# Performance work log

Hardware: AMD Instinct MI355X
Metric: run time of the kernel (lower is better)

Reference implementation:

```python
import jax, jax.numpy as jnp
import numpy as np

DIM = 512
HEADS = 8
DIM_HEAD = 64
H_DIM = HEADS * DIM_HEAD  # 512
SCALE = DIM_HEAD ** -0.5


def setup_inputs() -> dict:
    key = jax.random.key(0)
    k_x, k_qkv, k_out, k_b = jax.random.split(key, 4)
    N, C, L = 4, DIM, 2048
    x = jax.random.normal(k_x, (N, C, L), dtype=jnp.float32)
    # Conv1d kernel_size=1 weights, kernel dim squeezed: [out_ch, in_ch]
    w_qkv = jax.random.normal(k_qkv, (3 * H_DIM, DIM), dtype=jnp.float32) * (DIM ** -0.5)
    w_out = jax.random.normal(k_out, (DIM, H_DIM), dtype=jnp.float32) * (H_DIM ** -0.5)
    b_out = jax.random.normal(k_b, (DIM,), dtype=jnp.float32) * 0.01
    return {"x": x, "w_qkv": w_qkv, "w_out": w_out, "b_out": b_out}


def reference(x, w_qkv, w_out, b_out):
    N, C, L = x.shape
    # 1x1 conv == pointwise linear over channels
    qkv = jnp.einsum('oc,ncl->nol', w_qkv, x)            # N, 3*h_dim, L
    q, k, v = jnp.split(qkv, 3, axis=1)                  # each N, h_dim, L
    # split heads: N, h, d, L
    q = q.reshape(N, HEADS, DIM_HEAD, L) * SCALE
    k = k.reshape(N, HEADS, DIM_HEAD, L)
    v = v.reshape(N, HEADS, DIM_HEAD, L)
    sim = jnp.einsum('nhdi,nhdj->nhij', q, k)            # N, h, L, L
    attn = jax.nn.softmax(sim, axis=-1)                  # stable softmax (max-subtract fused)
    out = jnp.einsum('nhij,nhdj->nhid', attn, v)         # N, h, L, d
    # 'b h l c -> b (h c) l'
    out = jnp.transpose(out, (0, 1, 3, 2)).reshape(N, H_DIM, L)
    return jnp.einsum('oc,ncl->nol', w_out, out) + b_out[None, :, None]
```

## Files before the change

kernel.cpp:

```cpp
#include <hip/hip_runtime.h>
#include <hip/hip_bf16.h>
#include <stdint.h>
#include <stddef.h>

typedef unsigned short u16;
typedef __bf16 bf16x8 __attribute__((ext_vector_type(8)));
typedef __bf16 bf16x2 __attribute__((ext_vector_type(2)));
typedef float f32x4 __attribute__((ext_vector_type(4)));
typedef unsigned short u16x8 __attribute__((ext_vector_type(8)));
typedef unsigned short u16x4 __attribute__((ext_vector_type(4)));

#define NBATCH 4
#define LSEQ   2048
#define CDIM   512
#define NHEADS 8
#define DHEAD  64
#define QSCALE 0.18033688011112042f

__device__ __forceinline__ float exp2_hw(float x) {
  return __builtin_amdgcn_exp2f(x);
}

__device__ __forceinline__ u16 f2bf(float f) {
  union { float f; unsigned u; } v; v.f = f;
  return (u16)((v.u + 0x7FFFu + ((v.u >> 16) & 1u)) >> 16);
}
__device__ __forceinline__ u16 f2bf_hw(float f) {
  union { __bf16 b; u16 u; } cv; cv.b = (__bf16)f; return cv.u;
}
__device__ __forceinline__ unsigned pack2bf(float a, float b) {
  union { bf16x2 v; unsigned u; } cv;
  cv.v[0] = (__bf16)a; cv.v[1] = (__bf16)b;
  return cv.u;
}
__device__ __forceinline__ f32x4 mfma16(bf16x8 a, bf16x8 b, f32x4 c) {
  return __builtin_amdgcn_mfma_f32_16x16x32_bf16(a, b, c, 0, 0, 0);
}
__device__ __forceinline__ void async16(const u16* gp, const u16* lp) {
  auto* g = reinterpret_cast<const __attribute__((address_space(1))) uint32_t*>(
      reinterpret_cast<uintptr_t>(gp));
  auto* l = reinterpret_cast<__attribute__((address_space(3))) uint32_t*>(
      reinterpret_cast<uintptr_t>(lp));
  __builtin_amdgcn_global_load_lds(g, l, 16, 0, 0);
}

__global__ __launch_bounds__(256) void prep(const float* __restrict__ x,
                                            const float* __restrict__ wqkv,
                                            const float* __restrict__ wout,
                                            u16* __restrict__ xT,
                                            u16* __restrict__ wqkvb,
                                            u16* __restrict__ woutb) {
  __shared__ u16 tile[32][36];
  int b = blockIdx.x, t = threadIdx.x;
  if (b < 4096) {
    int lb = b & 63, cb = (b >> 6) & 15, n = b >> 10;
    int c = t >> 3, lq = (t & 7) * 4;
    float4 f = *(const float4*)(x + ((size_t)(n * CDIM + cb * 32 + c)) * LSEQ + lb * 32 + lq);
    u16x4 cv;
    cv[0] = f2bf(f.x); cv[1] = f2bf(f.y); cv[2] = f2bf(f.z); cv[3] = f2bf(f.w);
    *(u16x4*)&tile[c][lq] = cv;
    __syncthreads();
    int l = t >> 3, cq = (t & 7) * 4;
    u16x4 o;
    o[0] = tile[cq + 0][l]; o[1] = tile[cq + 1][l];
    o[2] = tile[cq + 2][l]; o[3] = tile[cq + 3][l];
    *(u16x4*)(xT + ((size_t)(n * LSEQ + lb * 32 + l)) * CDIM + cb * 32 + cq) = o;
  } else {
    int i = (b - 4096) * 256 + t;
    const float4* src;
    u16* dst;
    int idx;
    if (i < 196608) { src = (const float4*)wqkv; dst = wqkvb; idx = i; }
    else            { src = (const float4*)wout; dst = woutb; idx = i - 196608; }
    float4 f = src[idx];
    u16x4 o;
    o[0] = f2bf(f.x); o[1] = f2bf(f.y); o[2] = f2bf(f.z); o[3] = f2bf(f.w);
    *(u16x4*)(dst + (size_t)idx * 4) = o;
  }
}

__global__ __launch_bounds__(256, 3) void qkv_gemm(const u16* __restrict__ wqkvb,
                                                   const u16* __restrict__ xT,
                                                   u16* __restrict__ qT,
                                                   u16* __restrict__ kT,
                                                   u16* __restrict__ vp) {
  __shared__ __align__(16) u16 lds[17408];
  u16* At = lds;
  u16* Bt = lds + 8192;

  int mb = blockIdx.x, lb = blockIdx.y, n = blockIdx.z;
  int o0 = mb * 128, l0 = lb * 128;
  int t = threadIdx.x, w = t >> 6, lane = t & 63, quad = lane >> 4, l15 = lane & 15;
  int wr = w >> 1, wc = w & 1;
  int lr = lane >> 3, lc = lane & 7;
  int swzS = (lc ^ lr) * 8;
  int swzR = l15 & 7;

  const u16* ag = wqkvb + (size_t)(o0 + w * 32 + lr) * CDIM + swzS;
  const u16* bg = xT + ((size_t)n * LSEQ + l0 + w * 32 + lr) * CDIM + swzS;

  f32x4 acc[4][4];
#pragma unroll
  for (int i = 0; i < 4; ++i)
#pragma unroll
    for (int j = 0; j < 4; ++j) acc[i][j] = (f32x4)0.0f;

  for (int k0 = 0; k0 < CDIM; k0 += 64) {
#pragma unroll
    for (int g = 0; g < 4; ++g) {
      async16(ag + (size_t)g * 8 * CDIM + k0, At + (w * 32 + g * 8) * 64);
      async16(bg + (size_t)g * 8 * CDIM + k0, Bt + (w * 32 + g * 8) * 64);
    }
    __syncthreads();
    bf16x8 af[4][2], bf[4][2];
#pragma unroll
    for (int rt = 0; rt < 4; ++rt)
#pragma unroll
      for (int kk = 0; kk < 2; ++kk) {
        af[rt][kk] = *(const bf16x8*)&At[(wr * 64 + rt * 16 + l15) * 64 +
                                         (((kk * 4 + quad) ^ swzR) * 8)];
        bf[rt][kk] = *(const bf16x8*)&Bt[(wc * 64 + rt * 16 + l15) * 64 +
                                         (((kk * 4 + quad) ^ swzR) * 8)];
      }
#pragma unroll
    for (int kk = 0; kk < 2; ++kk)
#pragma unroll
      for (int rt = 0; rt < 4; ++rt)
#pragma unroll
        for (int ct = 0; ct < 4; ++ct)
          acc[rt][ct] = mfma16(af[rt][kk], bf[ct][kk], acc[rt][ct]);
    __syncthreads();
  }

  int seg = mb >> 2;
  int hb = (mb & 3) * 2;
  if (seg < 2) {
    float scale = (seg == 0) ? QSCALE : 1.0f;
#pragma unroll
    for (int rt = 0; rt < 4; ++rt)
#pragma unroll
      for (int ct = 0; ct < 4; ++ct) {
        u16x4 ov;
#pragma unroll
        for (int r = 0; r < 4; ++r) ov[r] = f2bf_hw(acc[rt][ct][r] * scale);
        *(u16x4*)&lds[(wc * 64 + ct * 16 + l15) * 136 + wr * 64 + rt * 16 + quad * 4] = ov;
      }
    __syncthreads();
    u16* dst0 = (seg == 0) ? qT : kT;
#pragma unroll
    for (int p = 0; p < 8; ++p) {
      int l = p * 16 + (t >> 4);
      int ch = t & 15;
      u16x8 val = *(const u16x8*)&lds[l * 136 + ch * 8];
      int h = hb + (ch >> 3);
      int d = (ch & 7) * 8;
      *(u16x8*)(dst0 + (((size_t)(n * NHEADS + h)) * LSEQ + l0 + l) * DHEAD + d) = val;
    }
  } else {
#pragma unroll
    for (int rt = 0; rt < 4; ++rt)
#pragma unroll
      for (int ct = 0; ct < 4; ++ct)
#pragma unroll
        for (int r = 0; r < 4; ++r)
          lds[(wr * 64 + rt * 16 + quad * 4 + r) * 136 + wc * 64 + ct * 16 + l15] =
              f2bf_hw(acc[rt][ct][r]);
    __syncthreads();
#pragma unroll
    for (int p = 0; p < 8; ++p) {
      int o = p * 16 + (t >> 4);
      int ch = t & 15;
      u16x8 val = *(const u16x8*)&lds[o * 136 + ch * 8];
      int h = hb + (o >> 6);
      int d = o & 63;
      *(u16x8*)(vp + (((size_t)(n * NHEADS + h)) * DHEAD + d) * LSEQ + l0 + ch * 8) = val;
    }
  }
}

__global__ __launch_bounds__(256, 2) void attn_kernel(const u16* __restrict__ qT,
                                                      const u16* __restrict__ kT,
                                                      const u16* __restrict__ vp,
                                                      u16* __restrict__ aoT) {
  __shared__ __align__(16) u16 KVs[3][8192];

  int ib = blockIdx.x, h = blockIdx.y, n = blockIdx.z;
  int i0 = ib * 128;
  const u16* qb = qT + ((size_t)(n * NHEADS + h)) * LSEQ * DHEAD;
  const u16* kb = kT + ((size_t)(n * NHEADS + h)) * LSEQ * DHEAD;
  const u16* vb = vp + ((size_t)(n * NHEADS + h)) * DHEAD * LSEQ;
  int t = threadIdx.x, w = t >> 6, lane = t & 63, quad = lane >> 4, l15 = lane & 15;
  int wi = w >> 1, wj = w & 1;

  bf16x8 qf[4][2];
#pragma unroll
  for (int it = 0; it < 4; ++it)
#pragma unroll
    for (int kk = 0; kk < 2; ++kk)
      qf[it][kk] = *(const bf16x8*)(qb + (size_t)(i0 + wi * 64 + it * 16 + l15) * DHEAD +
                                    kk * 32 + quad * 8);

  f32x4 Oc[4][4];
#pragma unroll
  for (int it = 0; it < 4; ++it)
#pragma unroll
    for (int dt = 0; dt < 4; ++dt) Oc[it][dt] = (f32x4)0.0f;
  float lsum[4] = {0.f, 0.f, 0.f, 0.f};

  int lr = lane >> 3, lc = lane & 7;
  int swz = lc ^ lr;
  const u16* kgl = kb + lr * DHEAD + swz * 8;
  const u16* vgl = vb + (size_t)lr * LSEQ + swz * 8;
  int swzK = l15 & 7;

  auto stage = [&](int j0, int b) {
#pragma unroll
    for (int s = 0; s < 2; ++s) {
      int g = s * 4 + w;
      async16(kgl + (size_t)j0 * DHEAD + g * 512, &KVs[b][g * 512]);
      async16(vgl + j0 + (size_t)g * 8 * LSEQ, &KVs[b][4096 + g * 512]);
    }
  };

  bf16x8 pf_c[4];
  bf16x8 vf_c[4];

  auto tile_body = [&](int tt, bool do_pv) {
    const u16* Kt = &KVs[tt % 3][0];
    const u16* Vt = &KVs[tt % 3][4096];

    bf16x8 kf[2][2];
#pragma unroll
    for (int jt = 0; jt < 2; ++jt)
#pragma unroll
      for (int kk = 0; kk < 2; ++kk)
        kf[jt][kk] = *(const bf16x8*)&Kt[(wj * 32 + 16 * jt + l15) * 64 +
                                         (((quad + 4 * kk) ^ swzK) * 8)];

    if (do_pv) {
#pragma unroll
      for (int it = 0; it < 4; ++it)
#pragma unroll
        for (int dt = 0; dt < 4; ++dt)
          Oc[it][dt] = mfma16(vf_c[dt], pf_c[it], Oc[it][dt]);
    }

    f32x4 st[4][2];
#pragma unroll
    for (int it = 0; it < 4; ++it)
#pragma unroll
      for (int jt = 0; jt < 2; ++jt) {
        f32x4 s = (f32x4)0.0f;
        s = mfma16(kf[jt][0], qf[it][0], s);
        s = mfma16(kf[jt][1], qf[it][1], s);
        st[it][jt] = s;
      }

#pragma unroll
    for (int dt = 0; dt < 4; ++dt)
      vf_c[dt] = *(const bf16x8*)&Vt[(16 * dt + l15) * 64 +
                                     (((wj * 4 + quad) ^ swzK) * 8)];

#pragma unroll
    for (int it = 0; it < 4; ++it) {
      unsigned wjh[2][2];
#pragma unroll
      for (int jt = 0; jt < 2; ++jt) {
        float p0 = exp2_hw(st[it][jt][0]);
        float p1 = exp2_hw(st[it][jt][1]);
        float p2 = exp2_hw(st[it][jt][2]);
        float p3 = exp2_hw(st[it][jt][3]);
        lsum[it] += (p0 + p1) + (p2 + p3);
        wjh[jt][0] = pack2bf(p0, p1);
        wjh[jt][1] = pack2bf(p2, p3);
      }
      unsigned a0 = wjh[0][0], b0 = wjh[1][0];
      unsigned a1 = wjh[0][1], b1 = wjh[1][1];
      asm volatile("v_permlane32_swap_b32 %0, %1" : "+v"(a0), "+v"(b0));
      asm volatile("v_permlane16_swap_b32 %0, %1" : "+v"(a0), "+v"(b0));
      asm volatile("v_permlane32_swap_b32 %0, %1" : "+v"(a1), "+v"(b1));
      asm volatile("v_permlane16_swap_b32 %0, %1" : "+v"(a1), "+v"(b1));
      union { unsigned u[4]; bf16x8 v; } cv;
      cv.u[0] = a0; cv.u[1] = a1; cv.u[2] = b0; cv.u[3] = b1;
      pf_c[it] = cv.v;
    }
  };

  stage(0, 0);
  stage(64, 1);

  asm volatile("s_waitcnt vmcnt(4)" ::: "memory");
  __builtin_amdgcn_s_barrier();
  __builtin_amdgcn_sched_barrier(0);
  stage(128, 2);
  tile_body(0, false);

  for (int tt = 1; tt < 31; ++tt) {
    asm volatile("s_waitcnt vmcnt(4)" ::: "memory");
    __builtin_amdgcn_s_barrier();
    __builtin_amdgcn_sched_barrier(0);
    if (tt + 2 < 32) stage((tt + 2) * 64, (tt + 2) % 3);
    tile_body(tt, true);
  }

  asm volatile("s_waitcnt vmcnt(0)" ::: "memory");
  __builtin_amdgcn_s_barrier();
  __builtin_amdgcn_sched_barrier(0);
  tile_body(31, true);

#pragma unroll
  for (int it = 0; it < 4; ++it)
#pragma unroll
    for (int dt = 0; dt < 4; ++dt)
      Oc[it][dt] = mfma16(vf_c[dt], pf_c[it], Oc[it][dt]);

#pragma unroll
  for (int it = 0; it < 4; ++it) {
    lsum[it] += __shfl_xor(lsum[it], 16, 64);
    lsum[it] += __shfl_xor(lsum[it], 32, 64);
  }
  __syncthreads();
  float* Os = (float*)&KVs[0][0];
  float* Ls = (float*)((char*)&KVs[0][0] + 40960);
  if (wj == 1) {
#pragma unroll
    for (int it = 0; it < 4; ++it) {
#pragma unroll
      for (int dt = 0; dt < 4; ++dt)
        *(f32x4*)&Os[((((wi * 4 + it) * 4 + dt) * 16) + l15) * 20 + 4 * quad] =
            Oc[it][dt];
      if (quad == 0) Ls[(wi * 4 + it) * 16 + l15] = lsum[it];
    }
  }
  __syncthreads();
  if (wj == 0) {
#pragma unroll
    for (int it = 0; it < 4; ++it) {
      float lt = lsum[it] + Ls[(wi * 4 + it) * 16 + l15];
      float inv = 1.0f / lt;
      int row = i0 + wi * 64 + it * 16 + l15;
#pragma unroll
      for (int dt = 0; dt < 4; ++dt) {
        f32x4 part = *(const f32x4*)&Os[((((wi * 4 + it) * 4 + dt) * 16) + l15) * 20 +
                                        4 * quad];
        u16x4 ov;
#pragma unroll
        for (int r = 0; r < 4; ++r)
          ov[r] = f2bf_hw((Oc[it][dt][r] + part[r]) * inv);
        *(u16x4*)(aoT + ((size_t)n * LSEQ + row) * CDIM + h * DHEAD + 16 * dt +
                  4 * quad) = ov;
      }
    }
  }
}

__global__ __launch_bounds__(256, 3) void out_gemm(const u16* __restrict__ woutb,
                                                   const u16* __restrict__ aoT,
                                                   const float* __restrict__ bout,
                                                   float* __restrict__ out) {
  __shared__ __align__(16) u16 lds[16384];
  u16* At = lds;
  u16* Bt = lds + 8192;

  int mb = blockIdx.x, lb = blockIdx.y, n = blockIdx.z;
  int o0 = mb * 128, l0 = lb * 128;
  int t = threadIdx.x, w = t >> 6, lane = t & 63, quad = lane >> 4, l15 = lane & 15;
  int wr = w >> 1, wc = w & 1;
  int lr = lane >> 3, lc = lane & 7;
  int swzS = (lc ^ lr) * 8;
  int swzR = l15 & 7;

  const u16* ag = woutb + (size_t)(o0 + w * 32 + lr) * CDIM + swzS;
  const u16* bg = aoT + ((size_t)n * LSEQ + l0 + w * 32 + lr) * CDIM + swzS;

  f32x4 acc[4][4];
#pragma unroll
  for (int i = 0; i < 4; ++i)
#pragma unroll
    for (int j = 0; j < 4; ++j) acc[i][j] = (f32x4)0.0f;

  for (int k0 = 0; k0 < CDIM; k0 += 64) {
#pragma unroll
    for (int g = 0; g < 4; ++g) {
      async16(ag + (size_t)g * 8 * CDIM + k0, At + (w * 32 + g * 8) * 64);
      async16(bg + (size_t)g * 8 * CDIM + k0, Bt + (w * 32 + g * 8) * 64);
    }
    __syncthreads();
    bf16x8 af[4][2], bf[4][2];
#pragma unroll
    for (int rt = 0; rt < 4; ++rt)
#pragma unroll
      for (int kk = 0; kk < 2; ++kk) {
        af[rt][kk] = *(const bf16x8*)&At[(wr * 64 + rt * 16 + l15) * 64 +
                                         (((kk * 4 + quad) ^ swzR) * 8)];
        bf[rt][kk] = *(const bf16x8*)&Bt[(wc * 64 + rt * 16 + l15) * 64 +
                                         (((kk * 4 + quad) ^ swzR) * 8)];
      }
#pragma unroll
    for (int kk = 0; kk < 2; ++kk)
#pragma unroll
      for (int rt = 0; rt < 4; ++rt)
#pragma unroll
        for (int ct = 0; ct < 4; ++ct)
          acc[rt][ct] = mfma16(af[rt][kk], bf[ct][kk], acc[rt][ct]);
    __syncthreads();
  }

#pragma unroll
  for (int rt = 0; rt < 4; ++rt) {
    int orow = o0 + wr * 64 + rt * 16 + quad * 4;
#pragma unroll
    for (int r = 0; r < 4; ++r) {
      float bb = bout[orow + r];
      float* orow_p = out + ((size_t)n * CDIM + orow + r) * LSEQ + l0 + wc * 64;
#pragma unroll
      for (int ct = 0; ct < 4; ++ct)
        orow_p[ct * 16 + l15] = acc[rt][ct][r] + bb;
    }
  }
}

extern "C" void kernel_launch(void* const* d_in, const int* in_sizes, int n_in,
                              void* d_out, int out_size, void* d_ws, size_t ws_size,
                              hipStream_t stream) {
  (void)in_sizes; (void)n_in; (void)out_size; (void)ws_size;
  const float* x    = (const float*)d_in[0];
  const float* wqkv = (const float*)d_in[1];
  const float* wout = (const float*)d_in[2];
  const float* bout = (const float*)d_in[3];

  char* ws = (char*)d_ws;
  u16* xT    = (u16*)(ws + 0);
  u16* wqkvb = (u16*)(ws + 8388608);
  u16* woutb = (u16*)(ws + 9961472);
  u16* qT    = (u16*)(ws + 10485760);
  u16* kT    = (u16*)(ws + 18874368);
  u16* vp    = (u16*)(ws + 27262976);
  u16* aoT   = (u16*)(ws + 35651584);

  hipLaunchKernelGGL(prep, dim3(5120), dim3(256), 0, stream, x, wqkv, wout, xT, wqkvb, woutb);
  hipLaunchKernelGGL(qkv_gemm, dim3(12, 16, 4), dim3(256), 0, stream, wqkvb, xT, qT, kT, vp);
  hipLaunchKernelGGL(attn_kernel, dim3(16, 8, 4), dim3(256), 0, stream, qT, kT, vp, aoT);
  hipLaunchKernelGGL(out_gemm, dim3(4, 16, 4), dim3(256), 0, stream, woutb, aoT, bout,
                     (float*)d_out);
}
```

Before: 148.5 us.

## Triple-buffer the output projection GEMM with async loads and manual waitcnt

The out_gemm K loop moves from a single LDS buffer with two barriers per step to a three-stage ring buffer. Global-to-LDS async loads for step ks+2 are issued while step ks computes, and explicit vmcnt waits plus a single barrier per step guard each buffer. This is meant to hide global load latency behind MFMA work. In exchange, LDS use per block triples and the launch-bounds occupancy hint is dropped, which may lower the number of resident blocks per CU.

```diff
diff --git a/kernel.cpp b/kernel.cpp
--- a/kernel.cpp
+++ b/kernel.cpp
@@ -354,13 +354,11 @@
   }
 }
 
-__global__ __launch_bounds__(256, 3) void out_gemm(const u16* __restrict__ woutb,
-                                                   const u16* __restrict__ aoT,
-                                                   const float* __restrict__ bout,
-                                                   float* __restrict__ out) {
-  __shared__ __align__(16) u16 lds[16384];
-  u16* At = lds;
-  u16* Bt = lds + 8192;
+__global__ __launch_bounds__(256) void out_gemm(const u16* __restrict__ woutb,
+                                                const u16* __restrict__ aoT,
+                                                const float* __restrict__ bout,
+                                                float* __restrict__ out) {
+  __shared__ __align__(16) u16 lds[49152];
 
   int mb = blockIdx.x, lb = blockIdx.y, n = blockIdx.z;
   int o0 = mb * 128, l0 = lb * 128;
@@ -379,13 +377,19 @@
 #pragma unroll
     for (int j = 0; j < 4; ++j) acc[i][j] = (f32x4)0.0f;
 
-  for (int k0 = 0; k0 < CDIM; k0 += 64) {
+  auto stage = [&](int ks, int b) {
+    u16* At = lds + b * 16384;
+    u16* Bt = At + 8192;
 #pragma unroll
     for (int g = 0; g < 4; ++g) {
-      async16(ag + (size_t)g * 8 * CDIM + k0, At + (w * 32 + g * 8) * 64);
-      async16(bg + (size_t)g * 8 * CDIM + k0, Bt + (w * 32 + g * 8) * 64);
-    }
-    __syncthreads();
+      async16(ag + (size_t)g * 8 * CDIM + ks * 64, At + (w * 32 + g * 8) * 64);
+      async16(bg + (size_t)g * 8 * CDIM + ks * 64, Bt + (w * 32 + g * 8) * 64);
+    }
+  };
+
+  auto body = [&](int ks) {
+    const u16* At = lds + (ks % 3) * 16384;
+    const u16* Bt = At + 8192;
     bf16x8 af[4][2], bf[4][2];
 #pragma unroll
     for (int rt = 0; rt < 4; ++rt)
@@ -403,8 +407,29 @@
 #pragma unroll
         for (int ct = 0; ct < 4; ++ct)
           acc[rt][ct] = mfma16(af[rt][kk], bf[ct][kk], acc[rt][ct]);
-    __syncthreads();
-  }
+  };
+
+  stage(0, 0);
+  stage(1, 1);
+
+  asm volatile("s_waitcnt vmcnt(8)" ::: "memory");
+  __builtin_amdgcn_s_barrier();
+  __builtin_amdgcn_sched_barrier(0);
+  stage(2, 2);
+  body(0);
+
+  for (int ks = 1; ks < 7; ++ks) {
+    asm volatile("s_waitcnt vmcnt(8)" ::: "memory");
+    __builtin_amdgcn_s_barrier();
+    __builtin_amdgcn_sched_barrier(0);
+    if (ks + 2 < 8) stage(ks + 2, (ks + 2) % 3);
+    body(ks);
+  }
+
+  asm volatile("s_waitcnt vmcnt(0)" ::: "memory");
+  __builtin_amdgcn_s_barrier();
+  __builtin_amdgcn_sched_barrier(0);
+  body(7);
 
 #pragma unroll
   for (int rt = 0; rt < 4; ++rt) {
```

Measured after the change: 143.3 us. 3.5% less time.
